# Optimization experiments

Hardware: AMD Instinct MI355X
Metric: run time of the kernel (lower is better)

Reference implementation:

```python
import jax, jax.numpy as jnp
import numpy as np

D_MODEL = 1024
N_HEADS = 16
D_KEYS = 64
D_LLM = 4096
Q_RANK = 512
KV_RANK = 512
EPS = 1e-5


def layernorm(x, g, b):
    mu = jnp.mean(x, axis=-1, keepdims=True)
    var = jnp.mean(jnp.square(x - mu), axis=-1, keepdims=True)
    return (x - mu) * jax.lax.rsqrt(var + EPS) * g + b


def setup_inputs() -> dict:
    key = jax.random.key(0)
    ks = jax.random.split(key, 10)
    te = jax.random.normal(ks[0], (4, 1024, D_MODEL), jnp.float32)
    se = jax.random.normal(ks[1], (1000, D_LLM), jnp.float32)
    s = 0.02
    return {
        'target_embedding': te,
        'source_embedding': se,
        'value_embedding': se,  # module asserts source == value
        'q_a_w': jax.random.normal(ks[2], (Q_RANK, D_MODEL), jnp.float32) * s,
        'q_ln_g': jnp.ones((Q_RANK,), jnp.float32),
        'q_ln_b': jnp.zeros((Q_RANK,), jnp.float32),
        'q_b_w': jax.random.normal(ks[3], (N_HEADS * D_KEYS, Q_RANK), jnp.float32) * s,
        'kv_a_w': jax.random.normal(ks[4], (KV_RANK, D_LLM), jnp.float32) * s,
        'kv_ln_g': jnp.ones((KV_RANK,), jnp.float32),
        'kv_ln_b': jnp.zeros((KV_RANK,), jnp.float32),
        'kv_b_w': jax.random.normal(ks[5], (N_HEADS * 2 * D_KEYS, KV_RANK), jnp.float32) * s,
        'out_w': jax.random.normal(ks[6], (D_LLM, N_HEADS * D_KEYS), jnp.float32) * s,
        'out_b': jnp.zeros((D_LLM,), jnp.float32),
    }


def reference(target_embedding, source_embedding, value_embedding,
              q_a_w, q_ln_g, q_ln_b, q_b_w,
              kv_a_w, kv_ln_g, kv_ln_b, kv_b_w, out_w, out_b):
    B, L, _ = target_embedding.shape
    S = source_embedding.shape[0]
    # Q path: LoRA down -> LN -> up, [B,L,H,E]
    q = layernorm(target_embedding @ q_a_w.T, q_ln_g, q_ln_b) @ q_b_w.T
    q = q.reshape(B, L, N_HEADS, D_KEYS)
    # KV path (no batch dim, broadcast across B)
    ckv = layernorm(source_embedding @ kv_a_w.T, kv_ln_g, kv_ln_b)  # [S, r]
    kv = (ckv @ kv_b_w.T).reshape(S, N_HEADS, 2 * D_KEYS)
    k, v = kv[..., :D_KEYS], kv[..., D_KEYS:]  # [S,H,E] each
    scale = 1.0 / np.sqrt(D_KEYS)
    scores = jnp.einsum('blhe,she->bhls', q, k)  # [B,H,L,S]
    A = jax.nn.softmax(scale * scores, axis=-1)  # dropout inactive (eval)
    out = jnp.einsum('bhls,she->blhe', A, v).reshape(B, L, N_HEADS * D_KEYS)
    return out @ out_w.T + out_b
```

## Files before the change

### kernel.cpp

```cpp
#include <hip/hip_runtime.h>

typedef unsigned short u16;
typedef __bf16 bf16x8 __attribute__((ext_vector_type(8)));
typedef __bf16 bf16x4 __attribute__((ext_vector_type(4)));
typedef float f32x4 __attribute__((ext_vector_type(4)));

#define DEV __device__ __forceinline__

DEV u16 f2bf(float f){
  unsigned u = __float_as_uint(f);
  u += 0x7fff + ((u >> 16) & 1);
  return (u16)(u >> 16);
}
DEV float bf2f(u16 v){ return __uint_as_float(((unsigned)v) << 16); }

DEV void gll16(const void* g, void* l){
  __builtin_amdgcn_global_load_lds(
    (__attribute__((address_space(1))) unsigned int*)(unsigned long long)g,
    (__attribute__((address_space(3))) unsigned int*)(unsigned int)(unsigned long long)l,
    16, 0, 0);
}

template<int WM, int WN, int OBF, int BIAS>
__global__ __launch_bounds__(256) void gemm_bt(
    const u16* __restrict__ A, int lda, long sA1, long sA2,
    const u16* __restrict__ B, int ldb, long sB1, long sB2,
    void* __restrict__ Cv, int ldc, long sC1, long sC2,
    const float* __restrict__ bias,
    int M, int N, int K, int Z2)
{
  constexpr int BM = WM*64, BN = WN*64;
  constexpr int NW = WM*WN;
  constexpr int A_INSTS = BM/16, B_INSTS = BN/16;
  constexpr int APW = A_INSTS/NW, BPW = B_INSTS/NW;
  __shared__ u16 sA[BM*32];
  __shared__ u16 sB[BN*32];
  const int tid  = threadIdx.x;
  const int wave = tid >> 6, lane = tid & 63;
  const int quad = lane >> 4, l16 = lane & 15;
  const int wm = wave % WM, wn = wave / WM;
  const long bm = blockIdx.y, bn = blockIdx.x;
  const int z  = blockIdx.z;
  const int z1 = z / Z2, z2 = z - z1*Z2;
  const u16* Ab = A + z1*sA1 + z2*sA2 + bm*BM*(long)lda;
  const u16* Bb = B + z1*sB1 + z2*sB2 + bn*BN*(long)ldb;

  f32x4 acc[4][4] = {};

  for (int k0 = 0; k0 < K; k0 += 32){
    __syncthreads();
#pragma unroll
    for (int j = 0; j < APW; j++){
      const int inst = wave*APW + j;
      const int o = inst*1024 + lane*16;
      const int row = o >> 6, colb = o & 63;
      gll16(Ab + (long)row*lda + k0 + (colb >> 1), &sA[inst*512]);
    }
#pragma unroll
    for (int j = 0; j < BPW; j++){
      const int inst = wave*BPW + j;
      const int o = inst*1024 + lane*16;
      const int row = o >> 6, colb = o & 63;
      gll16(Bb + (long)row*ldb + k0 + (colb >> 1), &sB[inst*512]);
    }
    __syncthreads();
    bf16x8 af[4], bfr[4];
#pragma unroll
    for (int mi = 0; mi < 4; mi++)
      af[mi] = *(const bf16x8*)&sA[(wm*64 + mi*16 + l16)*32 + quad*8];
#pragma unroll
    for (int ni = 0; ni < 4; ni++)
      bfr[ni] = *(const bf16x8*)&sB[(wn*64 + ni*16 + l16)*32 + quad*8];
#pragma unroll
    for (int mi = 0; mi < 4; mi++)
#pragma unroll
      for (int ni = 0; ni < 4; ni++)
        acc[mi][ni] = __builtin_amdgcn_mfma_f32_16x16x32_bf16(af[mi], bfr[ni], acc[mi][ni], 0, 0, 0);
  }

  const long crow0 = bm*BM + wm*64 + quad*4;
  const long ccol0 = bn*BN + wn*64 + l16;
  if (OBF){
    u16* Cp = (u16*)Cv + z1*sC1 + z2*sC2;
#pragma unroll
    for (int mi = 0; mi < 4; mi++)
#pragma unroll
      for (int ni = 0; ni < 4; ni++)
#pragma unroll
        for (int r = 0; r < 4; r++)
          Cp[(crow0 + mi*16 + r)*ldc + ccol0 + ni*16] = f2bf(acc[mi][ni][r]);
  } else {
    float* Cp = (float*)Cv + z1*sC1 + z2*sC2;
    float bv[4] = {0.f,0.f,0.f,0.f};
    if (BIAS){
#pragma unroll
      for (int ni = 0; ni < 4; ni++) bv[ni] = bias[ccol0 + ni*16];
    }
#pragma unroll
    for (int mi = 0; mi < 4; mi++)
#pragma unroll
      for (int ni = 0; ni < 4; ni++)
#pragma unroll
        for (int r = 0; r < 4; r++)
          Cp[(crow0 + mi*16 + r)*ldc + ccol0 + ni*16] = acc[mi][ni][r] + bv[ni];
  }
}

__global__ __launch_bounds__(512, 2) void gemm256(
    const u16* __restrict__ A, const u16* __restrict__ B,
    float* __restrict__ C, const float* __restrict__ bias,
    int N, int K, int TN)
{
  __shared__ __align__(16) u16 sA[32768];
  __shared__ __align__(16) u16 sB[32768];
  const int tid  = threadIdx.x;
  const int w    = tid >> 6, lane = tid & 63;
  const int quad = lane >> 4, l16 = lane & 15;
  const int wm = w >> 2, wn = w & 3;
  const int cpx = gridDim.x >> 3;
  const int bid = blockIdx.x;
  const int wg  = (bid & 7)*cpx + (bid >> 3);
  const long bm = wg / TN, bn = wg % TN;
  const int NT = K >> 6;

  const int rsub = lane >> 3;
  const int kk16 = (lane & 7) ^ rsub;
  const u16* Ag = A + (bm*256 + w*8 + rsub)*(long)K + kk16*8;
  const u16* Bg = B + (bn*256 + w*8 + rsub)*(long)K + kk16*8;
  u16* dA = sA + w*512;
  u16* dB = sB + w*512;

  auto stage = [&](const u16* G, u16* D, int T){
#pragma unroll
    for (int c = 0; c < 4; c++)
      gll16(G + ((long)c*64)*K + T*64, D + c*4096);
  };

  const int xr  = l16 & 7;
  const int ko0 = ((0*4 + quad) ^ xr) * 8;
  const int ko1 = ((1*4 + quad) ^ xr) * 8;
  const u16* rA0 = sA + (wm*128 + l16)*64;
  const u16* rB0 = sB + (wn*64  + l16)*64;

  f32x4 acc[8][4] = {};
  bf16x8 aF[4][2];

  stage(Ag, dA, 0);
  stage(Bg, dB, 0);
  asm volatile("s_waitcnt vmcnt(0)" ::: "memory");
  __builtin_amdgcn_s_barrier();

  for (int T = 0; T < NT; ++T){
    const int buf = T & 1;
    const u16* rA = rA0 + buf*16384;
    const u16* rB = rB0 + buf*16384;

    {
#pragma unroll
      for (int mi = 0; mi < 4; mi++){
        aF[mi][0] = *(const bf16x8*)(rA + mi*1024 + ko0);
        aF[mi][1] = *(const bf16x8*)(rA + mi*1024 + ko1);
      }
      bf16x8 bF[2][2];
#pragma unroll
      for (int ni = 0; ni < 2; ni++){
        bF[ni][0] = *(const bf16x8*)(rB + ni*1024 + ko0);
        bF[ni][1] = *(const bf16x8*)(rB + ni*1024 + ko1);
      }
      if (T+1 < NT){
        stage(Ag, dA + (buf^1)*16384, T+1);
        stage(Bg, dB + (buf^1)*16384, T+1);
      }
      __builtin_amdgcn_s_barrier();
      asm volatile("s_waitcnt lgkmcnt(0)" ::: "memory");
      __builtin_amdgcn_sched_barrier(0);
      __builtin_amdgcn_s_setprio(1);
#pragma unroll
      for (int kk = 0; kk < 2; kk++)
#pragma unroll
        for (int mi = 0; mi < 4; mi++)
#pragma unroll
          for (int ni = 0; ni < 2; ni++)
            acc[mi][ni] = __builtin_amdgcn_mfma_f32_16x16x32_bf16(aF[mi][kk], bF[ni][kk], acc[mi][ni], 0,0,0);
      __builtin_amdgcn_s_setprio(0);
      __builtin_amdgcn_s_barrier();
    }

    {
      bf16x8 bF[2][2];
#pragma unroll
      for (int ni = 0; ni < 2; ni++){
        bF[ni][0] = *(const bf16x8*)(rB + (2+ni)*1024 + ko0);
        bF[ni][1] = *(const bf16x8*)(rB + (2+ni)*1024 + ko1);
      }
      __builtin_amdgcn_s_barrier();
      asm volatile("s_waitcnt lgkmcnt(0)" ::: "memory");
      __builtin_amdgcn_sched_barrier(0);
      __builtin_amdgcn_s_setprio(1);
#pragma unroll
      for (int kk = 0; kk < 2; kk++)
#pragma unroll
        for (int mi = 0; mi < 4; mi++)
#pragma unroll
          for (int ni = 0; ni < 2; ni++)
            acc[mi][2+ni] = __builtin_amdgcn_mfma_f32_16x16x32_bf16(aF[mi][kk], bF[ni][kk], acc[mi][2+ni], 0,0,0);
      __builtin_amdgcn_s_setprio(0);
      __builtin_amdgcn_s_barrier();
    }

    {
#pragma unroll
      for (int mi = 0; mi < 4; mi++){
        aF[mi][0] = *(const bf16x8*)(rA + (4+mi)*1024 + ko0);
        aF[mi][1] = *(const bf16x8*)(rA + (4+mi)*1024 + ko1);
      }
      bf16x8 bF[2][2];
#pragma unroll
      for (int ni = 0; ni < 2; ni++){
        bF[ni][0] = *(const bf16x8*)(rB + ni*1024 + ko0);
        bF[ni][1] = *(const bf16x8*)(rB + ni*1024 + ko1);
      }
      __builtin_amdgcn_s_barrier();
      asm volatile("s_waitcnt lgkmcnt(0)" ::: "memory");
      __builtin_amdgcn_sched_barrier(0);
      __builtin_amdgcn_s_setprio(1);
#pragma unroll
      for (int kk = 0; kk < 2; kk++)
#pragma unroll
        for (int mi = 0; mi < 4; mi++)
#pragma unroll
          for (int ni = 0; ni < 2; ni++)
            acc[4+mi][ni] = __builtin_amdgcn_mfma_f32_16x16x32_bf16(aF[mi][kk], bF[ni][kk], acc[4+mi][ni], 0,0,0);
      __builtin_amdgcn_s_setprio(0);
      __builtin_amdgcn_s_barrier();
    }

    {
      bf16x8 bF[2][2];
#pragma unroll
      for (int ni = 0; ni < 2; ni++){
        bF[ni][0] = *(const bf16x8*)(rB + (2+ni)*1024 + ko0);
        bF[ni][1] = *(const bf16x8*)(rB + (2+ni)*1024 + ko1);
      }
      __builtin_amdgcn_s_barrier();
      asm volatile("s_waitcnt lgkmcnt(0)" ::: "memory");
      __builtin_amdgcn_sched_barrier(0);
      __builtin_amdgcn_s_setprio(1);
#pragma unroll
      for (int kk = 0; kk < 2; kk++)
#pragma unroll
        for (int mi = 0; mi < 4; mi++)
#pragma unroll
          for (int ni = 0; ni < 2; ni++)
            acc[4+mi][2+ni] = __builtin_amdgcn_mfma_f32_16x16x32_bf16(aF[mi][kk], bF[ni][kk], acc[4+mi][2+ni], 0,0,0);
      __builtin_amdgcn_s_setprio(0);
      asm volatile("s_waitcnt vmcnt(0)" ::: "memory");
      __builtin_amdgcn_s_barrier();
    }
  }

  const long crow0 = bm*256 + wm*128 + quad*4;
  const long ccol0 = bn*256 + wn*64  + l16;
  float bv[4];
#pragma unroll
  for (int ni = 0; ni < 4; ni++) bv[ni] = bias ? bias[ccol0 + ni*16] : 0.f;
#pragma unroll
  for (int mi = 0; mi < 8; mi++)
#pragma unroll
    for (int ni = 0; ni < 4; ni++)
#pragma unroll
      for (int r = 0; r < 4; r++)
        C[(crow0 + mi*16 + r)*(long)N + ccol0 + ni*16] = acc[mi][ni][r] + bv[ni];
}

__global__ __launch_bounds__(256) void cvt_all(
    const float* __restrict__ te,   const float* __restrict__ qaw,
    const float* __restrict__ qbw,  const float* __restrict__ kvaw,
    const float* __restrict__ kvbw, const float* __restrict__ outw,
    const float* __restrict__ se,
    u16* __restrict__ te_bf, u16* __restrict__ qa_bf, u16* __restrict__ qb_bf,
    u16* __restrict__ kva_bf, u16* __restrict__ kvb_bf,
    u16* __restrict__ outw_bf, u16* __restrict__ se_bf)
{
  const long NG = 4194304;
  for (long g = (long)blockIdx.x*256 + threadIdx.x; g < NG; g += (long)gridDim.x*256){
    const float* src; u16* dst; long rel; bool zero = false;
    if (g < 1048576)      { src=te;   dst=te_bf;   rel=g; }
    else if (g < 1179648) { src=qaw;  dst=qa_bf;   rel=g-1048576; }
    else if (g < 1310720) { src=qbw;  dst=qb_bf;   rel=g-1179648; }
    else if (g < 1835008) { src=kvaw; dst=kva_bf;  rel=g-1310720; }
    else if (g < 2097152) { src=kvbw; dst=kvb_bf;  rel=g-1835008; }
    else if (g < 3145728) { src=outw; dst=outw_bf; rel=g-2097152; }
    else                  { src=se;   dst=se_bf;   rel=g-3145728; zero = (rel>>10) >= 1000; }
    ushort4 o;
    if (!zero){
      float4 v = *(const float4*)(src + rel*4);
      o.x = f2bf(v.x); o.y = f2bf(v.y); o.z = f2bf(v.z); o.w = f2bf(v.w);
    } else { o.x = 0; o.y = 0; o.z = 0; o.w = 0; }
    *(ushort4*)(dst + rel*4) = o;
  }
}

__global__ __launch_bounds__(256) void ln_both(
    u16* __restrict__ out_q,  const float* __restrict__ in_q,
    const float* __restrict__ qg, const float* __restrict__ qb_,
    u16* __restrict__ out_kv, const float* __restrict__ in_kv,
    const float* __restrict__ kg, const float* __restrict__ kb_)
{
  long row; const float* in; u16* outp; const float* gam; const float* bet;
  int nparts; long pstride; int valid;
  if (blockIdx.x < 4096){
    row = blockIdx.x; in = in_q; outp = out_q; gam = qg; bet = qb_;
    nparts = 2; pstride = 4096L*512; valid = 1;
  } else {
    row = blockIdx.x - 4096; in = in_kv; outp = out_kv; gam = kg; bet = kb_;
    nparts = 8; pstride = 1024L*512; valid = (row < 1000);
  }
  const int tid = threadIdx.x;
  u16* op = outp + row*512 + tid*2;
  if (!valid){
    ushort2 z; z.x = 0; z.y = 0;
    *(ushort2*)op = z;
    return;
  }
  float2 x; x.x = 0.f; x.y = 0.f;
  for (int p = 0; p < nparts; p++){
    float2 v = *(const float2*)(in + p*pstride + row*512 + tid*2);
    x.x += v.x; x.y += v.y;
  }
  float s  = x.x + x.y;
  float s2 = x.x*x.x + x.y*x.y;
#pragma unroll
  for (int m = 32; m; m >>= 1){ s += __shfl_xor(s, m, 64); s2 += __shfl_xor(s2, m, 64); }
  __shared__ float red[8];
  const int wave = tid >> 6, lane = tid & 63;
  if (lane == 0){ red[wave*2] = s; red[wave*2+1] = s2; }
  __syncthreads();
  float ts = red[0]+red[2]+red[4]+red[6];
  float t2 = red[1]+red[3]+red[5]+red[7];
  float mu  = ts * (1.f/512.f);
  float var = t2 * (1.f/512.f) - mu*mu;
  float rs  = rsqrtf(var + 1e-5f);
  float2 g2 = *(const float2*)(gam + tid*2);
  float2 b2 = *(const float2*)(bet + tid*2);
  ushort2 o;
  o.x = f2bf((x.x - mu)*rs*g2.x + b2.x);
  o.y = f2bf((x.y - mu)*rs*g2.y + b2.y);
  *(ushort2*)op = o;
}

__global__ __launch_bounds__(256) void split_kv(
    const float* __restrict__ kv, u16* __restrict__ kbf, u16* __restrict__ vT)
{
  const int h  = blockIdx.x;
  const int sc = blockIdx.y;
  const int s0 = sc*64;
  const long PST = 1024L*2048;
  __shared__ u16 tile[64][65];
  const int e  = threadIdx.x & 63;
  const int sg = threadIdx.x >> 6;
#pragma unroll
  for (int i = 0; i < 16; i++){
    const int sl = i*4 + sg;
    const int s = s0 + sl;
    float kvl = kv[(long)s*2048 + h*128 + e]      + kv[PST + (long)s*2048 + h*128 + e];
    float vvl = kv[(long)s*2048 + h*128 + 64 + e] + kv[PST + (long)s*2048 + h*128 + 64 + e];
    kbf[((long)h*1024 + s)*64 + ((e + 8*s) & 63)] = f2bf(kvl);
    tile[sl][e] = f2bf(vvl);
  }
  __syncthreads();
#pragma unroll
  for (int i = 0; i < 16; i++){
    const int er = i*4 + sg;
    const int s  = s0 + e;
    const int t128 = s >> 7, pos = s & 127;
    vT[(((long)h*8 + t128)*64 + er)*128 + ((pos + 8*er) & 127)] = tile[e][er];
  }
}

__global__ __launch_bounds__(256) void flash_attn(
    const u16* __restrict__ Q, const u16* __restrict__ Kt,
    const u16* __restrict__ Vt, u16* __restrict__ O)
{
  __shared__ u16 sK[128*64];
  __shared__ u16 sV[64*128];
  __shared__ u16 sPT[128*136];
  __shared__ __align__(16) float sAl[128];
  const int tid = threadIdx.x, w = tid >> 6, lane = tid & 63;
  const int quad = lane >> 4, l16 = lane & 15;
  const int h = blockIdx.y;
  const long q0 = (long)blockIdx.x * 128;
  constexpr float SC = 0.18033688011f;

  bf16x8 bq[2][2];
#pragma unroll
  for (int ni = 0; ni < 2; ni++)
#pragma unroll
    for (int kf = 0; kf < 2; kf++)
      bq[ni][kf] = *(const bf16x8*)&Q[(q0 + w*32 + ni*16 + l16)*1024 + h*64 + kf*32 + quad*8];

  f32x4 accO[2][4] = {};
  float mst[2] = {-3e38f, -3e38f};
  float lst[2] = {0.f, 0.f};

#pragma unroll
  for (int j = 0; j < 4; j++){
    const int inst = w*4 + j;
    gll16(Kt + (long)h*65536 + inst*512 + lane*8, &sK[inst*512]);
  }
  __syncthreads();

  for (int it = 0; it < 8; it++){
#pragma unroll
    for (int j = 0; j < 4; j++){
      const int inst = w*4 + j;
      gll16(Vt + ((long)(h*8 + it))*8192 + inst*512 + lane*8, &sV[inst*512]);
    }

    f32x4 accS[8][2] = {};
#pragma unroll
    for (int kf = 0; kf < 2; kf++)
#pragma unroll
      for (int mi = 0; mi < 8; mi++){
        const int sr = mi*16 + l16;
        bf16x8 ka = *(const bf16x8*)&sK[sr*64 + ((kf*32 + quad*8 + 8*sr) & 63)];
#pragma unroll
        for (int ni = 0; ni < 2; ni++)
          accS[mi][ni] = __builtin_amdgcn_mfma_f32_16x16x32_bf16(ka, bq[ni][kf], accS[mi][ni], 0, 0, 0);
      }

    __syncthreads();

    if (it < 7){
      const long kb = (long)h*65536 + (long)(it+1)*128*64;
#pragma unroll
      for (int j = 0; j < 4; j++){
        const int inst = w*4 + j;
        gll16(Kt + kb + inst*512 + lane*8, &sK[inst*512]);
      }
    }

#pragma unroll
    for (int ni = 0; ni < 2; ni++){
#pragma unroll
      for (int mi = 0; mi < 8; mi++)
#pragma unroll
        for (int r = 0; r < 4; r++)
          accS[mi][ni][r] *= SC;
      if (it == 7){
#pragma unroll
        for (int mi = 0; mi < 8; mi++)
#pragma unroll
          for (int r = 0; r < 4; r++){
            const int s = 896 + mi*16 + quad*4 + r;
            if (s >= 1000) accS[mi][ni][r] = -3e38f;
          }
      }
      float m8[8];
#pragma unroll
      for (int mi = 0; mi < 8; mi++)
        m8[mi] = fmaxf(fmaxf(accS[mi][ni][0], accS[mi][ni][1]),
                       fmaxf(accS[mi][ni][2], accS[mi][ni][3]));
      float tm = fmaxf(fmaxf(fmaxf(m8[0], m8[1]), fmaxf(m8[2], m8[3])),
                       fmaxf(fmaxf(m8[4], m8[5]), fmaxf(m8[6], m8[7])));
      tm = fmaxf(tm, __shfl_xor(tm, 16, 64));
      tm = fmaxf(tm, __shfl_xor(tm, 32, 64));
      const float mnew = fmaxf(mst[ni], tm);
      const float al = exp2f(mst[ni] - mnew);
      mst[ni] = mnew;
      float sum = 0.f;
      const int qloc = w*32 + ni*16 + l16;
#pragma unroll
      for (int mi = 0; mi < 8; mi++){
        float p0 = exp2f(accS[mi][ni][0] - mnew);
        float p1 = exp2f(accS[mi][ni][1] - mnew);
        float p2 = exp2f(accS[mi][ni][2] - mnew);
        float p3 = exp2f(accS[mi][ni][3] - mnew);
        sum += (p0 + p1) + (p2 + p3);
        bf16x4 pk;
        pk[0] = (__bf16)p0; pk[1] = (__bf16)p1;
        pk[2] = (__bf16)p2; pk[3] = (__bf16)p3;
        *(bf16x4*)&sPT[qloc*136 + mi*16 + quad*4] = pk;
      }
      sum += __shfl_xor(sum, 16, 64);
      sum += __shfl_xor(sum, 32, 64);
      lst[ni] = lst[ni]*al + sum;
      if (quad == 0) sAl[qloc] = al;
    }

#pragma unroll
    for (int mi = 0; mi < 2; mi++){
      f32x4 al4 = *(const f32x4*)&sAl[w*32 + mi*16 + quad*4];
#pragma unroll
      for (int ni = 0; ni < 4; ni++)
        accO[mi][ni] *= al4;
    }

#pragma unroll
    for (int kf = 0; kf < 4; kf++){
      bf16x8 pa[2], vb[4];
#pragma unroll
      for (int mi = 0; mi < 2; mi++)
        pa[mi] = *(const bf16x8*)&sPT[(w*32 + mi*16 + l16)*136 + kf*32 + quad*8];
#pragma unroll
      for (int ni = 0; ni < 4; ni++){
        const int e = ni*16 + l16;
        vb[ni] = *(const bf16x8*)&sV[e*128 + ((kf*32 + quad*8 + 8*e) & 127)];
      }
#pragma unroll
      for (int mi = 0; mi < 2; mi++)
#pragma unroll
        for (int ni = 0; ni < 4; ni++)
          accO[mi][ni] = __builtin_amdgcn_mfma_f32_16x16x32_bf16(pa[mi], vb[ni], accO[mi][ni], 0, 0, 0);
    }
    __syncthreads();
  }

  if (quad == 0){ sAl[w*32 + l16] = lst[0]; sAl[w*32 + 16 + l16] = lst[1]; }
#pragma unroll
  for (int mi = 0; mi < 2; mi++){
    f32x4 l4 = *(const f32x4*)&sAl[w*32 + mi*16 + quad*4];
#pragma unroll
    for (int ni = 0; ni < 4; ni++)
#pragma unroll
      for (int r = 0; r < 4; r++)
        O[(q0 + w*32 + mi*16 + quad*4 + r)*1024 + h*64 + ni*16 + l16] =
            f2bf(accO[mi][ni][r] / l4[r]);
  }
}

extern "C" void kernel_launch(void* const* d_in, const int* in_sizes, int n_in,
                              void* d_out, int out_size, void* d_ws, size_t ws_size,
                              hipStream_t stream)
{
  const float* te   = (const float*)d_in[0];
  const float* se   = (const float*)d_in[1];
  const float* qaw  = (const float*)d_in[3];
  const float* qlg  = (const float*)d_in[4];
  const float* qlb  = (const float*)d_in[5];
  const float* qbw  = (const float*)d_in[6];
  const float* kvaw = (const float*)d_in[7];
  const float* kvlg = (const float*)d_in[8];
  const float* kvlb = (const float*)d_in[9];
  const float* kvbw = (const float*)d_in[10];
  const float* outw = (const float*)d_in[11];
  const float* outb = (const float*)d_in[12];
  float* out = (float*)d_out;
  (void)ws_size; (void)in_sizes; (void)n_in; (void)out_size;

  char* ws = (char*)d_ws;
  const size_t MB = 1024*1024;
  u16*   te_bf  = (u16*)  (ws + 0*MB);
  u16*   se_bf  = (u16*)  (ws + 8*MB);
  float* qlat   = (float*)(ws + 16*MB);
  float* ckvp   = (float*)(ws + 32*MB);
  float* kvf    = (float*)(ws + 48*MB);
  u16*   qa_bf   = (u16*)(ws + 64*MB);
  u16*   qb_bf   = (u16*)(ws + 65*MB);
  u16*   kva_bf  = (u16*)(ws + 66*MB);
  u16*   kvb_bf  = (u16*)(ws + 70*MB);
  u16*   outw_bf = (u16*)(ws + 72*MB);
  u16*   qln_bf  = (u16*)(ws + 80*MB);
  u16*   q_bf    = (u16*)(ws + 84*MB);
  u16*   ckv_bf  = (u16*)(ws + 92*MB);
  u16*   k_bf    = (u16*)(ws + 93*MB);
  u16*   vT_bf   = (u16*)(ws + 95*MB);
  u16*   attn_bf = (u16*)(ws + 97*MB);

  cvt_all<<<4096, 256, 0, stream>>>(
      te, qaw, qbw, kvaw, kvbw, outw, se,
      te_bf, qa_bf, qb_bf, kva_bf, kvb_bf, outw_bf, se_bf);

  gemm_bt<2,2,0,0><<<dim3(4, 32, 2), 256, 0, stream>>>(
      te_bf, 1024, 512, 0, qa_bf, 1024, 512, 0,
      qlat, 512, 4096L*512, 0, nullptr, 4096, 512, 512, 1);
  gemm_bt<2,2,0,0><<<dim3(4, 8, 8), 256, 0, stream>>>(
      se_bf, 4096, 512, 0, kva_bf, 4096, 512, 0,
      ckvp, 512, 1024L*512, 0, nullptr, 1024, 512, 512, 1);
  ln_both<<<4096 + 1024, 256, 0, stream>>>(
      qln_bf, qlat, qlg, qlb, ckv_bf, ckvp, kvlg, kvlb);
  gemm_bt<2,2,1,0><<<dim3(8, 32, 1), 256, 0, stream>>>(
      qln_bf, 512, 0,0, qb_bf, 512, 0,0, q_bf, 1024, 0,0, nullptr, 4096, 1024, 512, 1);
  gemm_bt<2,2,0,0><<<dim3(16, 8, 2), 256, 0, stream>>>(
      ckv_bf, 512, 256, 0, kvb_bf, 512, 256, 0,
      kvf, 2048, 1024L*2048, 0, nullptr, 1024, 2048, 256, 1);
  split_kv<<<dim3(16, 16), 256, 0, stream>>>(kvf, k_bf, vT_bf);

  flash_attn<<<dim3(32, 16), 256, 0, stream>>>(q_bf, k_bf, vT_bf, attn_bf);

  gemm256<<<dim3(256), 512, 0, stream>>>(
      attn_bf, outw_bf, out, outb, 4096, 1024, 16);
}
```

Before: 313.9 us.

## Shrink flash-attention tile, keep P in registers via shuffles, fold scale into weights

The flash attention kernel now gives each block 64 query rows instead of 128, one 16-row fragment per wave, and launches twice as many blocks with a 4-blocks-per-CU launch bound. The softmax probabilities no longer go through shared memory. They are moved into the PV MFMA operand layout with cross-lane shuffles, and the per-row alpha and l values are broadcast by shuffles instead of through LDS. The softmax scale is folded into the bf16 conversion of q_b_w, so no per-element multiply is needed. This cuts LDS traffic and raises occupancy, but each block loads K and V again with half as many queries, and the shuffles add ALU work.

```diff
diff --git a/kernel.cpp b/kernel.cpp
--- a/kernel.cpp
+++ b/kernel.cpp
@@ -283,11 +283,12 @@
     u16* __restrict__ outw_bf, u16* __restrict__ se_bf)
 {
   const long NG = 4194304;
+  const float QSC = 0.18033688011f;
   for (long g = (long)blockIdx.x*256 + threadIdx.x; g < NG; g += (long)gridDim.x*256){
-    const float* src; u16* dst; long rel; bool zero = false;
+    const float* src; u16* dst; long rel; bool zero = false; float sc = 1.f;
     if (g < 1048576)      { src=te;   dst=te_bf;   rel=g; }
     else if (g < 1179648) { src=qaw;  dst=qa_bf;   rel=g-1048576; }
-    else if (g < 1310720) { src=qbw;  dst=qb_bf;   rel=g-1179648; }
+    else if (g < 1310720) { src=qbw;  dst=qb_bf;   rel=g-1179648; sc = QSC; }
     else if (g < 1835008) { src=kvaw; dst=kva_bf;  rel=g-1310720; }
     else if (g < 2097152) { src=kvbw; dst=kvb_bf;  rel=g-1835008; }
     else if (g < 3145728) { src=outw; dst=outw_bf; rel=g-2097152; }
@@ -295,7 +296,7 @@
     ushort4 o;
     if (!zero){
       float4 v = *(const float4*)(src + rel*4);
-      o.x = f2bf(v.x); o.y = f2bf(v.y); o.z = f2bf(v.z); o.w = f2bf(v.w);
+      o.x = f2bf(v.x*sc); o.y = f2bf(v.y*sc); o.z = f2bf(v.z*sc); o.w = f2bf(v.w*sc);
     } else { o.x = 0; o.y = 0; o.z = 0; o.w = 0; }
     *(ushort4*)(dst + rel*4) = o;
   }
@@ -378,30 +379,25 @@
   }
 }
 
-__global__ __launch_bounds__(256) void flash_attn(
+__global__ __launch_bounds__(256, 4) void flash_attn(
     const u16* __restrict__ Q, const u16* __restrict__ Kt,
     const u16* __restrict__ Vt, u16* __restrict__ O)
 {
   __shared__ u16 sK[128*64];
   __shared__ u16 sV[64*128];
-  __shared__ u16 sPT[128*136];
-  __shared__ __align__(16) float sAl[128];
   const int tid = threadIdx.x, w = tid >> 6, lane = tid & 63;
   const int quad = lane >> 4, l16 = lane & 15;
   const int h = blockIdx.y;
-  const long q0 = (long)blockIdx.x * 128;
-  constexpr float SC = 0.18033688011f;
-
-  bf16x8 bq[2][2];
-#pragma unroll
-  for (int ni = 0; ni < 2; ni++)
-#pragma unroll
-    for (int kf = 0; kf < 2; kf++)
-      bq[ni][kf] = *(const bf16x8*)&Q[(q0 + w*32 + ni*16 + l16)*1024 + h*64 + kf*32 + quad*8];
-
-  f32x4 accO[2][4] = {};
-  float mst[2] = {-3e38f, -3e38f};
-  float lst[2] = {0.f, 0.f};
+  const long q0 = (long)blockIdx.x * 64;
+
+  bf16x8 bq[2];
+#pragma unroll
+  for (int kf = 0; kf < 2; kf++)
+    bq[kf] = *(const bf16x8*)&Q[(q0 + w*16 + l16)*1024 + h*64 + kf*32 + quad*8];
+
+  f32x4 accO[4] = {};
+  float mst = -3e38f;
+  float lst = 0.f;
 
 #pragma unroll
   for (int j = 0; j < 4; j++){
@@ -417,22 +413,20 @@
       gll16(Vt + ((long)(h*8 + it))*8192 + inst*512 + lane*8, &sV[inst*512]);
     }
 
-    f32x4 accS[8][2] = {};
+    f32x4 accS[8] = {};
 #pragma unroll
     for (int kf = 0; kf < 2; kf++)
 #pragma unroll
       for (int mi = 0; mi < 8; mi++){
         const int sr = mi*16 + l16;
         bf16x8 ka = *(const bf16x8*)&sK[sr*64 + ((kf*32 + quad*8 + 8*sr) & 63)];
-#pragma unroll
-        for (int ni = 0; ni < 2; ni++)
-          accS[mi][ni] = __builtin_amdgcn_mfma_f32_16x16x32_bf16(ka, bq[ni][kf], accS[mi][ni], 0, 0, 0);
+        accS[mi] = __builtin_amdgcn_mfma_f32_16x16x32_bf16(ka, bq[kf], accS[mi], 0, 0, 0);
       }
 
     __syncthreads();
 
     if (it < 7){
-      const long kb = (long)h*65536 + (long)(it+1)*128*64;
+      const long kb = (long)h*65536 + (long)(it+1)*8192;
 #pragma unroll
       for (int j = 0; j < 4; j++){
         const int inst = w*4 + j;
@@ -440,93 +434,83 @@
       }
     }
 
-#pragma unroll
-    for (int ni = 0; ni < 2; ni++){
+    if (it == 7){
 #pragma unroll
       for (int mi = 0; mi < 8; mi++)
 #pragma unroll
-        for (int r = 0; r < 4; r++)
-          accS[mi][ni][r] *= SC;
-      if (it == 7){
-#pragma unroll
-        for (int mi = 0; mi < 8; mi++)
-#pragma unroll
-          for (int r = 0; r < 4; r++){
-            const int s = 896 + mi*16 + quad*4 + r;
-            if (s >= 1000) accS[mi][ni][r] = -3e38f;
-          }
-      }
-      float m8[8];
-#pragma unroll
-      for (int mi = 0; mi < 8; mi++)
-        m8[mi] = fmaxf(fmaxf(accS[mi][ni][0], accS[mi][ni][1]),
-                       fmaxf(accS[mi][ni][2], accS[mi][ni][3]));
-      float tm = fmaxf(fmaxf(fmaxf(m8[0], m8[1]), fmaxf(m8[2], m8[3])),
-                       fmaxf(fmaxf(m8[4], m8[5]), fmaxf(m8[6], m8[7])));
-      tm = fmaxf(tm, __shfl_xor(tm, 16, 64));
-      tm = fmaxf(tm, __shfl_xor(tm, 32, 64));
-      const float mnew = fmaxf(mst[ni], tm);
-      const float al = exp2f(mst[ni] - mnew);
-      mst[ni] = mnew;
-      float sum = 0.f;
-      const int qloc = w*32 + ni*16 + l16;
-#pragma unroll
-      for (int mi = 0; mi < 8; mi++){
-        float p0 = exp2f(accS[mi][ni][0] - mnew);
-        float p1 = exp2f(accS[mi][ni][1] - mnew);
-        float p2 = exp2f(accS[mi][ni][2] - mnew);
-        float p3 = exp2f(accS[mi][ni][3] - mnew);
-        sum += (p0 + p1) + (p2 + p3);
-        bf16x4 pk;
-        pk[0] = (__bf16)p0; pk[1] = (__bf16)p1;
-        pk[2] = (__bf16)p2; pk[3] = (__bf16)p3;
-        *(bf16x4*)&sPT[qloc*136 + mi*16 + quad*4] = pk;
-      }
-      sum += __shfl_xor(sum, 16, 64);
-      sum += __shfl_xor(sum, 32, 64);
-      lst[ni] = lst[ni]*al + sum;
-      if (quad == 0) sAl[qloc] = al;
-    }
-
-#pragma unroll
-    for (int mi = 0; mi < 2; mi++){
-      f32x4 al4 = *(const f32x4*)&sAl[w*32 + mi*16 + quad*4];
-#pragma unroll
-      for (int ni = 0; ni < 4; ni++)
-        accO[mi][ni] *= al4;
-    }
+        for (int r = 0; r < 4; r++){
+          const int s = 896 + mi*16 + quad*4 + r;
+          if (s >= 1000) accS[mi][r] = -3e38f;
+        }
+    }
+    float m8[8];
+#pragma unroll
+    for (int mi = 0; mi < 8; mi++)
+      m8[mi] = fmaxf(fmaxf(accS[mi][0], accS[mi][1]),
+                     fmaxf(accS[mi][2], accS[mi][3]));
+    float tm = fmaxf(fmaxf(fmaxf(m8[0], m8[1]), fmaxf(m8[2], m8[3])),
+                     fmaxf(fmaxf(m8[4], m8[5]), fmaxf(m8[6], m8[7])));
+    tm = fmaxf(tm, __shfl_xor(tm, 16, 64));
+    tm = fmaxf(tm, __shfl_xor(tm, 32, 64));
+    const float mnew = fmaxf(mst, tm);
+    const float al = exp2f(mst - mnew);
+    mst = mnew;
+    float sum = 0.f;
+    unsigned du[8][2];
+#pragma unroll
+    for (int mi = 0; mi < 8; mi++){
+      float p0 = exp2f(accS[mi][0] - mnew);
+      float p1 = exp2f(accS[mi][1] - mnew);
+      float p2 = exp2f(accS[mi][2] - mnew);
+      float p3 = exp2f(accS[mi][3] - mnew);
+      sum += (p0 + p1) + (p2 + p3);
+      union { bf16x4 v; unsigned u[2]; } pk;
+      pk.v[0] = (__bf16)p0; pk.v[1] = (__bf16)p1;
+      pk.v[2] = (__bf16)p2; pk.v[3] = (__bf16)p3;
+      du[mi][0] = pk.u[0]; du[mi][1] = pk.u[1];
+    }
+    sum += __shfl_xor(sum, 16, 64);
+    sum += __shfl_xor(sum, 32, 64);
+    lst = lst*al + sum;
+
+    f32x4 al4;
+#pragma unroll
+    for (int r = 0; r < 4; r++) al4[r] = __shfl(al, quad*4 + r, 64);
+#pragma unroll
+    for (int ni = 0; ni < 4; ni++) accO[ni] *= al4;
 
 #pragma unroll
     for (int kf = 0; kf < 4; kf++){
-      bf16x8 pa[2], vb[4];
-#pragma unroll
-      for (int mi = 0; mi < 2; mi++)
-        pa[mi] = *(const bf16x8*)&sPT[(w*32 + mi*16 + l16)*136 + kf*32 + quad*8];
+      union { unsigned u[4]; bf16x8 v; } pa;
+#pragma unroll
+      for (int jj = 0; jj < 4; jj++){
+        const int src = l16 + ((lane & 16) << 1) + ((jj >> 1) << 4);
+        const unsigned a0 = __shfl(du[2*kf    ][jj & 1], src, 64);
+        const unsigned a1 = __shfl(du[2*kf + 1][jj & 1], src, 64);
+        pa.u[jj] = (quad < 2) ? a0 : a1;
+      }
+      bf16x8 vb[4];
 #pragma unroll
       for (int ni = 0; ni < 4; ni++){
         const int e = ni*16 + l16;
         vb[ni] = *(const bf16x8*)&sV[e*128 + ((kf*32 + quad*8 + 8*e) & 127)];
       }
 #pragma unroll
-      for (int mi = 0; mi < 2; mi++)
-#pragma unroll
-        for (int ni = 0; ni < 4; ni++)
-          accO[mi][ni] = __builtin_amdgcn_mfma_f32_16x16x32_bf16(pa[mi], vb[ni], accO[mi][ni], 0, 0, 0);
+      for (int ni = 0; ni < 4; ni++)
+        accO[ni] = __builtin_amdgcn_mfma_f32_16x16x32_bf16(pa.v, vb[ni], accO[ni], 0, 0, 0);
     }
     __syncthreads();
   }
 
-  if (quad == 0){ sAl[w*32 + l16] = lst[0]; sAl[w*32 + 16 + l16] = lst[1]; }
-#pragma unroll
-  for (int mi = 0; mi < 2; mi++){
-    f32x4 l4 = *(const f32x4*)&sAl[w*32 + mi*16 + quad*4];
-#pragma unroll
-    for (int ni = 0; ni < 4; ni++)
-#pragma unroll
-      for (int r = 0; r < 4; r++)
-        O[(q0 + w*32 + mi*16 + quad*4 + r)*1024 + h*64 + ni*16 + l16] =
-            f2bf(accO[mi][ni][r] / l4[r]);
-  }
+  f32x4 l4;
+#pragma unroll
+  for (int r = 0; r < 4; r++) l4[r] = __shfl(lst, quad*4 + r, 64);
+#pragma unroll
+  for (int ni = 0; ni < 4; ni++)
+#pragma unroll
+    for (int r = 0; r < 4; r++)
+      O[(q0 + w*16 + quad*4 + r)*1024 + h*64 + ni*16 + l16] =
+          f2bf(accO[ni][r] / l4[r]);
 }
 
 extern "C" void kernel_launch(void* const* d_in, const int* in_sizes, int n_in,
@@ -586,7 +570,7 @@
       kvf, 2048, 1024L*2048, 0, nullptr, 1024, 2048, 256, 1);
   split_kv<<<dim3(16, 16), 256, 0, stream>>>(kvf, k_bf, vT_bf);
 
-  flash_attn<<<dim3(32, 16), 256, 0, stream>>>(q_bf, k_bf, vT_bf, attn_bf);
+  flash_attn<<<dim3(64, 16), 256, 0, stream>>>(q_bf, k_bf, vT_bf, attn_bf);
 
   gemm256<<<dim3(256), 512, 0, stream>>>(
       attn_bf, outw_bf, out, outb, 4096, 1024, 16);
```

After: 312.1 us. No clear change (-0.6%).
